# Kernel optimization log

Measured on AMD Instinct MI355X. Metric: run time of the kernel, lower is better.

## Reference

```python
import jax, jax.numpy as jnp
import numpy as np

NUM_CLASSES = 5
TEMPERATURE = 3.0
BATCH = 4_194_304


def setup_inputs() -> dict:
    key = jax.random.key(0)
    k1, k2 = jax.random.split(key)
    quality_score = jax.random.uniform(k1, (BATCH,), dtype=jnp.float32)
    class_logits = jax.random.normal(k2, (BATCH, NUM_CLASSES), dtype=jnp.float32)
    return {"quality_score": quality_score, "class_logits": class_logits}


def _soft_targets(score, num_classes):
    # Vectorized version of the per-sample python loop in the torch module.
    C = num_classes
    # int(clamp(score*C, 0, C-1)) -> floor for non-negative scores
    idx = jnp.floor(jnp.clip(score * C, 0.0, C - 1)).astype(jnp.int32)
    center = (idx.astype(score.dtype) + 0.5) / C
    dist = jnp.abs(score - center) * C
    cond_lo = (idx > 0) & (score < center)          # spill to class idx-1
    cond_hi = (idx < C - 1) & (score > center)      # spill to class idx+1
    has_nb = cond_lo | cond_hi
    main_val = jnp.where(has_nb, 1.0 - dist, 1.0)
    nb_idx = idx - cond_lo.astype(jnp.int32) + cond_hi.astype(jnp.int32)
    nb_val = jnp.where(has_nb, dist, 0.0)
    cols = jnp.arange(C)
    # [B, C] dense soft targets built by broadcasted one-hot masks (no scatter)
    soft = (main_val[:, None] * (cols[None, :] == idx[:, None])
            + nb_val[:, None] * (cols[None, :] == nb_idx[:, None]))
    return soft


def reference(quality_score, class_logits):
    T = TEMPERATURE
    C = class_logits.shape[-1]
    B = class_logits.shape[0]
    soft = _soft_targets(quality_score, C)
    p = jax.nn.softmax(soft / T, axis=-1)               # targets (probs)
    logq = jax.nn.log_softmax(class_logits / T, axis=-1)
    # F.kl_div(logq, p, reduction='batchmean') = sum p*(log p - logq) / B
    kl = jnp.sum(p * (jnp.log(p) - logq)) / B
    return kl * T * T
```

## Files before the change

kernel.cpp:

```cpp
#include <hip/hip_runtime.h>
#include <math.h>


constexpr int   kC     = 5;
constexpr float kInvT  = 1.0f / 3.0f;
constexpr float kExp13 = 1.3956124250860895f;
constexpr int   kBatch = 4194304;

constexpr int kThreads        = 256;
constexpr int kQuadsPerThread = 2;
constexpr int kQuadsPerBlock  = kThreads * kQuadsPerThread;
constexpr int kBlocks         = (kBatch / 4) / kQuadsPerBlock;

__device__ __forceinline__ float kl_quad(float4 P0, float4 P1, float4 P2,
                                         float4 P3, float4 P4, float4 s4) {
    const float v[20] = {P0.x, P0.y, P0.z, P0.w,
                         P1.x, P1.y, P1.z, P1.w,
                         P2.x, P2.y, P2.z, P2.w,
                         P3.x, P3.y, P3.z, P3.w,
                         P4.x, P4.y, P4.z, P4.w};
    const float ss[4] = {s4.x, s4.y, s4.z, s4.w};

    float acc = 0.0f;
    #pragma unroll
    for (int r = 0; r < 4; ++r) {
        const float s  = ss[r];
        const float l0 = v[r * 5 + 0], l1 = v[r * 5 + 1], l2 = v[r * 5 + 2],
                    l3 = v[r * 5 + 3], l4 = v[r * 5 + 4];

        const float sc     = fminf(fmaxf(s * 5.0f, 0.0f), 4.0f);
        const int   idx    = (int)sc;
        const float center = ((float)idx + 0.5f) * 0.2f;
        float       d      = fabsf(s - center) * 5.0f;
        const bool  lo     = (idx > 0) && (s < center);
        const bool  hi     = (idx < kC - 1) && (s > center);
        const bool  nb     = lo || hi;
        d = nb ? d : 0.0f;
        const int nbi = idx + (hi ? 1 : 0) - (lo ? 1 : 0);

        const float e_nb   = __expf(d * kInvT);
        const float e_main = kExp13 * __builtin_amdgcn_rcpf(e_nb);

        const float S = l0 + l1 + l2 + l3 + l4;
        const float l_main = (idx == 0) ? l0 : (idx == 1) ? l1 :
                             (idx == 2) ? l2 : (idx == 3) ? l3 : l4;
        const float l_nb   = (nbi == 0) ? l0 : (nbi == 1) ? l1 :
                             (nbi == 2) ? l2 : (nbi == 3) ? l3 : l4;

        const float Zq = __expf(l0 * kInvT) + __expf(l1 * kInvT) +
                         __expf(l2 * kInvT) + __expf(l3 * kInvT) +
                         __expf(l4 * kInvT);

        const float Zp  = e_main + e_nb + 3.0f;
        const float rZp = __builtin_amdgcn_rcpf(Zp);
        const float Spa = e_main * (1.0f - d) + e_nb * d;
        const float Spl = e_main * l_main + e_nb * l_nb + (S - l_main - l_nb);

        acc += kInvT * (Spa - Spl) * rZp + __logf(Zq * rZp);
    }
    return acc;
}

__global__ __launch_bounds__(kThreads) void kl_partial_kernel(
    const float* __restrict__ score,
    const float* __restrict__ logits,
    float* __restrict__ partial) {

    const int t = threadIdx.x;
    const int wave = t >> 6;
    const int lane = t & 63;

    const size_t qA = (size_t)blockIdx.x * kQuadsPerBlock + t;
    const size_t qB = qA + kThreads;

    const float4* __restrict__ glog = reinterpret_cast<const float4*>(logits);
    const float4* __restrict__ gsc  = reinterpret_cast<const float4*>(score);

    const size_t aA = qA * 5, aB = qB * 5;
    const float4 A0 = glog[aA + 0], A1 = glog[aA + 1], A2 = glog[aA + 2],
                 A3 = glog[aA + 3], A4 = glog[aA + 4];
    const float4 B0 = glog[aB + 0], B1 = glog[aB + 1], B2 = glog[aB + 2],
                 B3 = glog[aB + 3], B4 = glog[aB + 4];
    const float4 sA = gsc[qA];
    const float4 sB = gsc[qB];

    float acc = kl_quad(A0, A1, A2, A3, A4, sA)
              + kl_quad(B0, B1, B2, B3, B4, sB);

    #pragma unroll
    for (int off = 32; off > 0; off >>= 1) acc += __shfl_down(acc, off, 64);

    __shared__ float wsum[kThreads / 64];
    if (lane == 0) wsum[wave] = acc;
    __syncthreads();
    if (t == 0) {
        float b = 0.0f;
        #pragma unroll
        for (int w = 0; w < kThreads / 64; ++w) b += wsum[w];
        partial[blockIdx.x] = b;
    }
}

__global__ __launch_bounds__(256) void kl_final_kernel(
    const float* __restrict__ partial,
    float* __restrict__ out) {
    const int t = threadIdx.x;
    const float4* p4 = reinterpret_cast<const float4*>(partial);
    const float4 a = p4[t], b = p4[t + 256];
    float acc = a.x + a.y + a.z + a.w + b.x + b.y + b.z + b.w;

    #pragma unroll
    for (int off = 32; off > 0; off >>= 1) acc += __shfl_down(acc, off, 64);

    __shared__ float wsum[4];
    if ((t & 63) == 0) wsum[t >> 6] = acc;
    __syncthreads();
    if (t == 0) {
        out[0] = (wsum[0] + wsum[1] + wsum[2] + wsum[3]) * (9.0f / (float)kBatch);
    }
}

extern "C" void kernel_launch(void* const* d_in, const int* in_sizes, int n_in,
                              void* d_out, int out_size, void* d_ws, size_t ws_size,
                              hipStream_t stream) {
    const float* score  = (const float*)d_in[0];
    const float* logits = (const float*)d_in[1];
    float* out     = (float*)d_out;
    float* partial = (float*)d_ws;

    kl_partial_kernel<<<kBlocks, kThreads, 0, stream>>>(score, logits, partial);
    kl_final_kernel<<<1, 256, 0, stream>>>(partial, out);
}
```

Measured before the change: 136.0 us.

## Stage logits through LDS with direct global-to-LDS loads, one quad per thread

```diff
diff --git a/kernel.cpp b/kernel.cpp
--- a/kernel.cpp
+++ b/kernel.cpp
@@ -7,10 +7,9 @@
 constexpr float kExp13 = 1.3956124250860895f;
 constexpr int   kBatch = 4194304;
 
-constexpr int kThreads        = 256;
-constexpr int kQuadsPerThread = 2;
-constexpr int kQuadsPerBlock  = kThreads * kQuadsPerThread;
-constexpr int kBlocks         = (kBatch / 4) / kQuadsPerBlock;
+constexpr int kThreads       = 256;
+constexpr int kQuadsPerBlock = kThreads;
+constexpr int kBlocks        = (kBatch / 4) / kQuadsPerBlock;
 
 __device__ __forceinline__ float kl_quad(float4 P0, float4 P1, float4 P2,
                                          float4 P3, float4 P4, float4 s4) {
@@ -66,26 +65,32 @@
     const float* __restrict__ logits,
     float* __restrict__ partial) {
 
-    const int t = threadIdx.x;
+    __shared__ float4 slog4[4 * 320];
+
+    const int t    = threadIdx.x;
     const int wave = t >> 6;
     const int lane = t & 63;
 
-    const size_t qA = (size_t)blockIdx.x * kQuadsPerBlock + t;
-    const size_t qB = qA + kThreads;
+    const size_t q = (size_t)blockIdx.x * kQuadsPerBlock + t;
 
-    const float4* __restrict__ glog = reinterpret_cast<const float4*>(logits);
-    const float4* __restrict__ gsc  = reinterpret_cast<const float4*>(score);
+    const float4* gsrc = reinterpret_cast<const float4*>(logits)
+                       + (size_t)blockIdx.x * (kQuadsPerBlock * 5)
+                       + wave * 320;
+    #pragma unroll
+    for (int j = 0; j < 5; ++j) {
+        __builtin_amdgcn_global_load_lds(
+            (const __attribute__((address_space(1))) void*)(gsrc + j * 64 + lane),
+            (__attribute__((address_space(3))) void*)(&slog4[wave * 320 + j * 64]),
+            16, 0, 0);
+    }
 
-    const size_t aA = qA * 5, aB = qB * 5;
-    const float4 A0 = glog[aA + 0], A1 = glog[aA + 1], A2 = glog[aA + 2],
-                 A3 = glog[aA + 3], A4 = glog[aA + 4];
-    const float4 B0 = glog[aB + 0], B1 = glog[aB + 1], B2 = glog[aB + 2],
-                 B3 = glog[aB + 3], B4 = glog[aB + 4];
-    const float4 sA = gsc[qA];
-    const float4 sB = gsc[qB];
+    const float4 sA = reinterpret_cast<const float4*>(score)[q];
 
-    float acc = kl_quad(A0, A1, A2, A3, A4, sA)
-              + kl_quad(B0, B1, B2, B3, B4, sB);
+    asm volatile("s_waitcnt vmcnt(0)" ::: "memory");
+
+    const int a0 = wave * 320 + lane * 5;
+    float acc = kl_quad(slog4[a0], slog4[a0 + 1], slog4[a0 + 2],
+                        slog4[a0 + 3], slog4[a0 + 4], sA);
 
     #pragma unroll
     for (int off = 32; off > 0; off >>= 1) acc += __shfl_down(acc, off, 64);
@@ -106,8 +111,9 @@
     float* __restrict__ out) {
     const int t = threadIdx.x;
     const float4* p4 = reinterpret_cast<const float4*>(partial);
-    const float4 a = p4[t], b = p4[t + 256];
-    float acc = a.x + a.y + a.z + a.w + b.x + b.y + b.z + b.w;
+    const float4 a = p4[t], b = p4[t + 256], c = p4[t + 512], d = p4[t + 768];
+    float acc = a.x + a.y + a.z + a.w + b.x + b.y + b.z + b.w
+              + c.x + c.y + c.z + c.w + d.x + d.y + d.z + d.w;
 
     #pragma unroll
     for (int off = 32; off > 0; off >>= 1) acc += __shfl_down(acc, off, 64);
```

After: 136.6 us. No clear change (+0.4%).
